# Performance work log

Hardware: AMD Instinct MI355X
Metric: run time of the kernel (lower is better)

## Reference

```python
import jax, jax.numpy as jnp
import numpy as np
import math

B, S, D = 1, 4096, 1024
H = 16
HD = D // H  # 64
MUP_SCALE = math.sqrt(1024 / 1024)  # mup_base_d_model defaults to d_in -> 1.0
ROPE_BASE = 10000.0


def apply_rope(x):
    # x: [B, H, S, HD], interleaved-pair RoPE (torchtune style)
    s, hd = x.shape[-2], x.shape[-1]
    inv_freq = 1.0 / (ROPE_BASE ** (jnp.arange(0, hd, 2, dtype=jnp.float32) / hd))  # [HD/2]
    ang = jnp.arange(s, dtype=jnp.float32)[:, None] * inv_freq[None, :]  # [S, HD/2]
    cos, sin = jnp.cos(ang), jnp.sin(ang)
    xp = x.reshape(*x.shape[:-1], hd // 2, 2)  # [..., HD/2, 2]
    x1, x2 = xp[..., 0], xp[..., 1]
    r1 = x1 * cos - x2 * sin
    r2 = x1 * sin + x2 * cos
    return jnp.stack([r1, r2], axis=-1).reshape(x.shape).astype(x.dtype)


def setup_inputs() -> dict:
    key = jax.random.key(0)
    ks = jax.random.split(key, 6)
    std = 1.0 / math.sqrt(D)
    x = jax.random.normal(ks[0], (B, S, D), dtype=jnp.float32)
    Wq = jax.random.normal(ks[1], (D, D), dtype=jnp.float32) * std  # torch layout [d_out, d_in]
    Wk = jax.random.normal(ks[2], (D, D), dtype=jnp.float32) * std
    Wv = jax.random.normal(ks[3], (D, D), dtype=jnp.float32) * std
    Wo = jax.random.normal(ks[4], (D, D), dtype=jnp.float32) * std
    bo = jnp.zeros((D,), dtype=jnp.float32)
    return {"x": x, "Wq": Wq, "Wk": Wk, "Wv": Wv, "Wo": Wo, "bo": bo}


def reference(x, Wq, Wk, Wv, Wo, bo):
    b, s, _ = x.shape
    q = jnp.einsum('bsd,ed->bse', x, Wq).reshape(b, s, H, HD).transpose(0, 2, 1, 3)
    k = jnp.einsum('bsd,ed->bse', x, Wk).reshape(b, s, H, HD).transpose(0, 2, 1, 3)
    v = jnp.einsum('bsd,ed->bse', x, Wv).reshape(b, s, H, HD).transpose(0, 2, 1, 3)
    q = apply_rope(q)
    k = apply_rope(k)
    scale = math.sqrt(HD) * MUP_SCALE
    scores = jnp.einsum('bhqd,bhkd->bhqk', q, k) / scale  # [B,H,S,S]
    causal = jnp.tril(jnp.ones((s, s), dtype=bool))
    scores = jnp.where(causal, scores, -jnp.inf)
    attn = jax.nn.softmax(scores, axis=-1)  # dropout p=0.0 -> identity
    ctx = jnp.einsum('bhqk,bhkd->bhqd', attn, v)
    ctx = ctx.transpose(0, 2, 1, 3).reshape(b, s, D)
    return jnp.einsum('bsd,ed->bse', ctx, Wo) + bo
```

## Files before the change

kernel.cpp:

```cpp
#include <hip/hip_runtime.h>
#include <hip/hip_bf16.h>

typedef __hip_bfloat16 bf16;
typedef unsigned short u16;
typedef unsigned int u32;
typedef float f32x4 __attribute__((ext_vector_type(4)));
typedef float f32x16 __attribute__((ext_vector_type(16)));
typedef __bf16 bf16x8 __attribute__((ext_vector_type(8)));
typedef u16 u16x8 __attribute__((ext_vector_type(8)));

#define DMODEL 1024
#define NH 16
#define HD 64
#define QK_LD 2048
#define SLEN 4096

typedef __attribute__((address_space(1))) const void* as1_cvp;
typedef __attribute__((address_space(3))) void* as3_vp;

__device__ __forceinline__ void gload_lds16(const void* g, void* l) {
  __builtin_amdgcn_global_load_lds((as1_cvp)g, (as3_vp)l, 16, 0, 0);
}

__device__ __forceinline__ f32x4 mfma16(bf16x8 a, bf16x8 b, f32x4 c) {
  return __builtin_amdgcn_mfma_f32_16x16x32_bf16(a, b, c, 0, 0, 0);
}
__device__ __forceinline__ f32x16 mfma32(bf16x8 a, bf16x8 b, f32x16 c) {
  return __builtin_amdgcn_mfma_f32_32x32x16_bf16(a, b, c, 0, 0, 0);
}

__device__ __forceinline__ float fexp2(float x) {
#if __has_builtin(__builtin_amdgcn_exp2f)
  return __builtin_amdgcn_exp2f(x);
#else
  return __expf(x * 0.6931471805599453f);
#endif
}

__device__ __forceinline__ u16 f2b(float f) {
  union { bf16 b; u16 s; } u; u.b = __float2bfloat16(f); return u.s;
}
__device__ __forceinline__ u32 pkbf(float a, float b) {
  union { __hip_bfloat162 h; u32 u; } cv;
  cv.h = __float22bfloat162_rn(make_float2(a, b));
  return cv.u;
}

__global__ __launch_bounds__(256) void cvt_kernel(const float* __restrict__ src,
                                                  bf16* __restrict__ dst, int n) {
  int i = (blockIdx.x * 256 + threadIdx.x) * 4;
  if (i >= n) return;
  float4 v = *(const float4*)(src + i);
  union { ushort4 u; bf16 h[4]; } o;
  o.h[0] = __float2bfloat16(v.x);
  o.h[1] = __float2bfloat16(v.y);
  o.h[2] = __float2bfloat16(v.z);
  o.h[3] = __float2bfloat16(v.w);
  *(ushort4*)(dst + i) = o.u;
}

__global__ __launch_bounds__(256) void rope_kernel(bf16* __restrict__ qk) {
  int idx = blockIdx.x * 256 + threadIdx.x;
  int p = idx & 511;
  int s = (idx >> 9) & 4095;
  int region = idx >> 21;
  int i = p & 31;
  int h = p >> 5;
  long base = (long)s * QK_LD + region * DMODEL + h * HD + 2 * i;
  float x1 = __bfloat162float(qk[base]);
  float x2 = __bfloat162float(qk[base + 1]);
  float invf = powf(10000.0f, -(float)(2 * i) / 64.0f);
  float ang = (float)s * invf;
  float sn, cs;
  sincosf(ang, &sn, &cs);
  float scale = (region == 0) ? 0.18033688011112042f : 1.0f;
  float r1 = (x1 * cs - x2 * sn) * scale;
  float r2 = (x1 * sn + x2 * cs) * scale;
  qk[base]     = __float2bfloat16(r1);
  qk[base + 1] = __float2bfloat16(r2);
}

template <int OUT_BF16>
__global__ __launch_bounds__(256) void gemm_bt(const bf16* __restrict__ A,
                                               const bf16* __restrict__ B,
                                               void* __restrict__ Cout,
                                               const float* __restrict__ bias,
                                               int M, int N, int K) {
  __shared__ __align__(16) bf16 As[128 * 32];
  __shared__ __align__(16) bf16 Bs[128 * 32];
  const int tid = threadIdx.x;
  const int lane = tid & 63;
  const int wid = tid >> 6;
  const int brow = blockIdx.y * 128;
  const int bcol = blockIdx.x * 128;
  const int wr = wid >> 1, wc = wid & 1;

  f32x4 acc[4][4] = {};

  const int srow = lane >> 2;
  const int scol = (lane & 3) * 8;
  const bf16* Ag = A + (long)(brow + wid * 32 + srow) * K + scol;
  const bf16* Bg = B + (long)(bcol + wid * 32 + srow) * K + scol;
  bf16* AsW = As + wid * 32 * 32;
  bf16* BsW = Bs + wid * 32 * 32;
  const int kof = (lane >> 4) * 8;
  const int r16 = lane & 15;

  for (int k0 = 0; k0 < K; k0 += 32) {
    __syncthreads();
    gload_lds16(Ag + k0, AsW);
    gload_lds16(Ag + k0 + (long)16 * K, AsW + 16 * 32);
    gload_lds16(Bg + k0, BsW);
    gload_lds16(Bg + k0 + (long)16 * K, BsW + 16 * 32);
    __syncthreads();
    bf16x8 af[4], bfr[4];
#pragma unroll
    for (int m = 0; m < 4; ++m)
      af[m] = *(const bf16x8*)(As + (wr * 64 + m * 16 + r16) * 32 + kof);
#pragma unroll
    for (int n = 0; n < 4; ++n)
      bfr[n] = *(const bf16x8*)(Bs + (wc * 64 + n * 16 + r16) * 32 + kof);
#pragma unroll
    for (int m = 0; m < 4; ++m)
#pragma unroll
      for (int n = 0; n < 4; ++n)
        acc[m][n] = mfma16(af[m], bfr[n], acc[m][n]);
  }

  const int r0 = (lane >> 4) * 4;
#pragma unroll
  for (int m = 0; m < 4; ++m) {
#pragma unroll
    for (int n = 0; n < 4; ++n) {
      int row = brow + wr * 64 + m * 16 + r0;
      int col = bcol + wc * 64 + n * 16 + r16;
#pragma unroll
      for (int r = 0; r < 4; ++r) {
        if (OUT_BF16) {
          ((bf16*)Cout)[(long)(row + r) * N + col] = __float2bfloat16(acc[m][n][r]);
        } else {
          ((float*)Cout)[(long)(row + r) * N + col] = acc[m][n][r] + bias[col];
        }
      }
    }
  }
}

__global__ __launch_bounds__(256, 4) void attn_kernel(const bf16* __restrict__ qk,
                                                      const bf16* __restrict__ vt,
                                                      bf16* __restrict__ ctx) {
  __shared__ __align__(16) bf16 smem[16384];
  bf16 (*Ks)[64][64] = (bf16(*)[64][64])(smem);
  bf16 (*Vt)[64][64] = (bf16(*)[64][64])(smem + 8192);

  const int tid = threadIdx.x;
  const int lane = tid & 63;
  const int wid = tid >> 6;
  const int hi = lane >> 5;
  const int l31 = lane & 31;
  const int t = blockIdx.x >> 4;
  const int h = blockIdx.x & 15;
  const int p = wid & 1;
  const int qblk = (wid < 2) ? (127 - t) : t;
  const int q0w = qblk * 32;
  const long kcol = DMODEL + (long)h * HD;

  bf16x8 qf[4];
  {
    const bf16* qp = qk + (long)(q0w + l31) * QK_LD + h * HD + hi * 8;
#pragma unroll
    for (int kt = 0; kt < 4; ++kt) qf[kt] = *(const bf16x8*)(qp + kt * 16);
  }

  const int kOff = ((lane & 7) ^ (lane >> 3)) * 8;
  const int lr = lane >> 3;
  const int srowp = (lr & 3) + 8 * (lr >> 2);

  int kro[4];
#pragma unroll
  for (int kt = 0; kt < 4; ++kt)
    kro[kt] = l31 * 64 + ((((kt << 1) | hi) ^ (l31 & 7)) * 8);
  const int vbase = l31 * 64;
  const int vslotx = l31 & 7;

  const bf16* vth = vt + (long)h * HD * SLEN;

  f32x16 acc[2] = {};
  float m_r = -1e30f, l_r = 0.0f;

  const int nkb = (129 - t) >> 1;
  const int vR = lane >> 3;

  {
#pragma unroll
    for (int c2 = 0; c2 < 2; ++c2) {
      const int c = wid * 2 + c2;
      const int sub = c >> 2, cc = c & 3;
      gload_lds16(qk + (long)(sub * 32 + srowp + 4 * (cc & 1) + 16 * (cc >> 1)) * QK_LD + kcol + kOff,
                  &Ks[0][c * 8][0]);
    }
#pragma unroll
    for (int c2 = 0; c2 < 2; ++c2) {
      const int d0 = wid * 16 + c2 * 8;
      gload_lds16(vth + (long)(d0 + vR) * SLEN + kOff, &Vt[0][d0][0]);
    }
  }

  for (int kb = 0; kb < nkb; ++kb) {
    const int cur = kb & 1;
    const int kvs = kb * 64 + p * 32;
    const bool pre = (kb + 1 < nkb);
    __syncthreads();

    if (pre) {
      const long kvn = (long)(kb + 1) * 64;
#pragma unroll
      for (int c2 = 0; c2 < 2; ++c2) {
        const int c = wid * 2 + c2;
        const int sub = c >> 2, cc = c & 3;
        gload_lds16(qk + (kvn + sub * 32 + srowp + 4 * (cc & 1) + 16 * (cc >> 1)) * QK_LD + kcol + kOff,
                    &Ks[cur ^ 1][c * 8][0]);
      }
#pragma unroll
      for (int c2 = 0; c2 < 2; ++c2) {
        const int d0 = wid * 16 + c2 * 8;
        gload_lds16(vth + (long)(d0 + vR) * SLEN + kvn + kOff, &Vt[cur ^ 1][d0][0]);
      }
    }

    if (kvs <= q0w + 31) {
      const bf16* KsC = &Ks[cur][0][0];
      const bf16* VtC = &Vt[cur][0][0];

      f32x16 c16 = {};
      __builtin_amdgcn_s_setprio(1);
#pragma unroll
      for (int kt = 0; kt < 4; ++kt) {
        bf16x8 kf = *(const bf16x8*)(KsC + p * 2048 + kro[kt]);
        c16 = mfma32(kf, qf[kt], c16);
      }
      __builtin_amdgcn_s_setprio(0);

      if (kvs + 31 > q0w) {
        const int q = q0w + l31;
        const int kvb = kvs + 8 * hi;
#pragma unroll
        for (int r = 0; r < 16; ++r) {
          int kv = kvb + (r & 3) + 4 * ((r >> 2) & 1) + 16 * (r >> 3);
          if (kv > q) c16[r] = -1e30f;
        }
      }

      float x0 = fmaxf(fmaxf(c16[0], c16[1]), fmaxf(c16[2], c16[3]));
      float x1 = fmaxf(fmaxf(c16[4], c16[5]), fmaxf(c16[6], c16[7]));
      float x2 = fmaxf(fmaxf(c16[8], c16[9]), fmaxf(c16[10], c16[11]));
      float x3 = fmaxf(fmaxf(c16[12], c16[13]), fmaxf(c16[14], c16[15]));
      float pmax = fmaxf(fmaxf(x0, x1), fmaxf(x2, x3));
      pmax = fmaxf(pmax, __shfl_xor(pmax, 32, 64));

      if (!__all(pmax <= m_r + 11.0f)) {
        float mn = fmaxf(m_r, pmax);
        float al = fexp2(m_r - mn);
        m_r = mn;
        l_r *= al;
#pragma unroll
        for (int dt = 0; dt < 2; ++dt)
#pragma unroll
          for (int r = 0; r < 16; ++r) acc[dt][r] *= al;
      }

      float pa[16];
#pragma unroll
      for (int r = 0; r < 16; ++r) pa[r] = fexp2(c16[r] - m_r);
      float rs = ((pa[0] + pa[1]) + (pa[2] + pa[3])) + ((pa[4] + pa[5]) + (pa[6] + pa[7])) +
                 (((pa[8] + pa[9]) + (pa[10] + pa[11])) + ((pa[12] + pa[13]) + (pa[14] + pa[15])));
      l_r += rs;

      union BP { u32 u[4]; bf16x8 v; } f0, f1;
      f0.u[0] = pkbf(pa[0], pa[1]);   f0.u[1] = pkbf(pa[2], pa[3]);
      f0.u[2] = pkbf(pa[4], pa[5]);   f0.u[3] = pkbf(pa[6], pa[7]);
      f1.u[0] = pkbf(pa[8], pa[9]);   f1.u[1] = pkbf(pa[10], pa[11]);
      f1.u[2] = pkbf(pa[12], pa[13]); f1.u[3] = pkbf(pa[14], pa[15]);

      __builtin_amdgcn_s_setprio(1);
#pragma unroll
      for (int dt = 0; dt < 2; ++dt) {
        const bf16* vrow = VtC + dt * 2048 + vbase;
        bf16x8 v0 = *(const bf16x8*)(vrow + (((p * 4 + hi) ^ vslotx) * 8));
        acc[dt] = mfma32(v0, f0.v, acc[dt]);
        bf16x8 v1 = *(const bf16x8*)(vrow + (((p * 4 + 2 + hi) ^ vslotx) * 8));
        acc[dt] = mfma32(v1, f1.v, acc[dt]);
      }
      __builtin_amdgcn_s_setprio(0);
    }
  }

  __syncthreads();
  float* fs = (float*)smem;
  if (wid & 1) {
    float* mb = fs + (wid >> 1) * 2176 + lane * 34;
#pragma unroll
    for (int dt = 0; dt < 2; ++dt)
#pragma unroll
      for (int r = 0; r < 16; ++r) mb[dt * 16 + r] = acc[dt][r];
    mb[32] = m_r;
    mb[33] = l_r;
  }
  __syncthreads();
  if (!(wid & 1)) {
    const float* mb = fs + (wid >> 1) * 2176 + lane * 34;
    float m1 = mb[32], l1 = mb[33];
    float ms = fmaxf(m_r, m1);
    float e0 = fexp2(m_r - ms), e1 = fexp2(m1 - ms);
    l_r = l_r * e0 + l1 * e1;
#pragma unroll
    for (int dt = 0; dt < 2; ++dt)
#pragma unroll
      for (int r = 0; r < 16; ++r)
        acc[dt][r] = acc[dt][r] * e0 + mb[dt * 16 + r] * e1;

    const float l_tot = l_r + __shfl_xor(l_r, 32, 64);
    const float inv = 1.0f / l_tot;
    bf16* scr = smem + 10240 + (wid >> 1) * 2176;
#pragma unroll
    for (int dt = 0; dt < 2; ++dt)
#pragma unroll
      for (int g2 = 0; g2 < 4; ++g2) {
        union { u16 hh[4]; unsigned long long q8; } pk4;
#pragma unroll
        for (int j = 0; j < 4; ++j) pk4.hh[j] = f2b(acc[dt][g2 * 4 + j] * inv);
        *(unsigned long long*)(scr + l31 * 68 + dt * 32 + g2 * 8 + 4 * hi) = pk4.q8;
      }
  }
  __syncthreads();
  if (!(wid & 1)) {
    const bf16* scr = smem + 10240 + (wid >> 1) * 2176;
    const int qe = lane >> 1, he = lane & 1;
    u16* cp = (u16*)ctx + (long)(q0w + qe) * DMODEL + h * HD + he * 32;
#pragma unroll
    for (int j = 0; j < 4; ++j) {
      u16x8 v = *(const u16x8*)(scr + qe * 68 + he * 32 + j * 8);
      *(u16x8*)(cp + j * 8) = v;
    }
  }
}

extern "C" void kernel_launch(void* const* d_in, const int* in_sizes, int n_in,
                              void* d_out, int out_size, void* d_ws, size_t ws_size,
                              hipStream_t stream) {
  (void)in_sizes; (void)n_in; (void)out_size; (void)ws_size;
  const float* x  = (const float*)d_in[0];
  const float* Wq = (const float*)d_in[1];
  const float* Wk = (const float*)d_in[2];
  const float* Wv = (const float*)d_in[3];
  const float* Wo = (const float*)d_in[4];
  const float* bo = (const float*)d_in[5];
  float* out = (float*)d_out;

  char* ws = (char*)d_ws;
  bf16* xb  = (bf16*)(ws);
  bf16* wqk = (bf16*)(ws + 8388608);
  bf16* wvb = (bf16*)(ws + 12582912);
  bf16* wob = (bf16*)(ws + 14680064);
  bf16* qkb = (bf16*)(ws + 16777216);
  bf16* vtb = (bf16*)(ws + 33554432);
  bf16* ctxb = (bf16*)(ws + 41943040);

  cvt_kernel<<<dim3(4096), dim3(256), 0, stream>>>(x, xb, 4194304);
  cvt_kernel<<<dim3(1024), dim3(256), 0, stream>>>(Wq, wqk, 1048576);
  cvt_kernel<<<dim3(1024), dim3(256), 0, stream>>>(Wk, wqk + 1048576, 1048576);
  cvt_kernel<<<dim3(1024), dim3(256), 0, stream>>>(Wv, wvb, 1048576);
  cvt_kernel<<<dim3(1024), dim3(256), 0, stream>>>(Wo, wob, 1048576);

  gemm_bt<1><<<dim3(16, 32), dim3(256), 0, stream>>>(xb, wqk, (void*)qkb, nullptr,
                                                     4096, 2048, 1024);
  gemm_bt<1><<<dim3(32, 8), dim3(256), 0, stream>>>(wvb, xb, (void*)vtb, nullptr,
                                                    1024, 4096, 1024);
  rope_kernel<<<dim3(16384), dim3(256), 0, stream>>>(qkb);
  attn_kernel<<<dim3(1024), dim3(256), 0, stream>>>(qkb, vtb, ctxb);
  gemm_bt<0><<<dim3(8, 32), dim3(256), 0, stream>>>(ctxb, wob, (void*)out, bo,
                                                    4096, 1024, 1024);
}
```

Baseline: 190.8 us.

## Merge convert and QKV GEMM launches, vectorize RoPE with precomputed trig table

Result: faster. 156.4 us (-18.0%).

```diff
diff --git a/kernel.cpp b/kernel.cpp
--- a/kernel.cpp
+++ b/kernel.cpp
@@ -46,10 +46,28 @@
   return cv.u;
 }
 
-__global__ __launch_bounds__(256) void cvt_kernel(const float* __restrict__ src,
-                                                  bf16* __restrict__ dst, int n) {
-  int i = (blockIdx.x * 256 + threadIdx.x) * 4;
-  if (i >= n) return;
+__global__ __launch_bounds__(256) void cvt5_kernel(const float* __restrict__ x,
+                                                   const float* __restrict__ wq,
+                                                   const float* __restrict__ wk,
+                                                   const float* __restrict__ wv,
+                                                   const float* __restrict__ wo,
+                                                   bf16* __restrict__ xb,
+                                                   bf16* __restrict__ wqk,
+                                                   bf16* __restrict__ wvb,
+                                                   bf16* __restrict__ wob) {
+  int bid = blockIdx.x;
+  const float* src; bf16* dst; long off;
+  if (bid < 4096) {
+    src = x; dst = xb; off = (long)bid * 1024;
+  } else {
+    int w = (bid - 4096) >> 10;
+    off = (long)((bid - 4096) & 1023) * 1024;
+    if (w == 0)      { src = wq; dst = wqk; }
+    else if (w == 1) { src = wk; dst = wqk + 1048576; }
+    else if (w == 2) { src = wv; dst = wvb; }
+    else             { src = wo; dst = wob; }
+  }
+  long i = off + threadIdx.x * 4;
   float4 v = *(const float4*)(src + i);
   union { ushort4 u; bf16 h[4]; } o;
   o.h[0] = __float2bfloat16(v.x);
@@ -59,25 +77,39 @@
   *(ushort4*)(dst + i) = o.u;
 }
 
-__global__ __launch_bounds__(256) void rope_kernel(bf16* __restrict__ qk) {
+__global__ __launch_bounds__(256) void trig_kernel(float2* __restrict__ tab) {
   int idx = blockIdx.x * 256 + threadIdx.x;
-  int p = idx & 511;
-  int s = (idx >> 9) & 4095;
-  int region = idx >> 21;
-  int i = p & 31;
-  int h = p >> 5;
-  long base = (long)s * QK_LD + region * DMODEL + h * HD + 2 * i;
-  float x1 = __bfloat162float(qk[base]);
-  float x2 = __bfloat162float(qk[base + 1]);
+  int s = idx >> 5, i = idx & 31;
   float invf = powf(10000.0f, -(float)(2 * i) / 64.0f);
   float ang = (float)s * invf;
   float sn, cs;
   sincosf(ang, &sn, &cs);
-  float scale = (region == 0) ? 0.18033688011112042f : 1.0f;
-  float r1 = (x1 * cs - x2 * sn) * scale;
-  float r2 = (x1 * sn + x2 * cs) * scale;
-  qk[base]     = __float2bfloat16(r1);
-  qk[base + 1] = __float2bfloat16(r2);
+  tab[idx] = make_float2(cs, sn);
+}
+
+__global__ __launch_bounds__(256) void rope_kernel(bf16* __restrict__ qk,
+                                                   const float2* __restrict__ tab) {
+  long e = (long)(blockIdx.x * 256 + threadIdx.x) * 8;
+  int s = (int)(e >> 11);
+  int col = (int)(e & 2047);
+  int i0 = (col & 63) >> 1;
+  float scale = (col < 1024) ? 0.18033688011112042f : 1.0f;
+  u16x8 v = *(const u16x8*)((const u16*)qk + e);
+  const float4* tp = (const float4*)(tab + s * 32 + i0);
+  float4 t0 = tp[0], t1 = tp[1];
+  float cs[4] = {t0.x, t0.z, t1.x, t1.z};
+  float sn[4] = {t0.y, t0.w, t1.y, t1.w};
+  u16x8 o;
+#pragma unroll
+  for (int j = 0; j < 4; ++j) {
+    union { u16 s; bf16 b; } a1, a2;
+    a1.s = v[2 * j]; a2.s = v[2 * j + 1];
+    float x1 = __bfloat162float(a1.b);
+    float x2 = __bfloat162float(a2.b);
+    o[2 * j]     = f2b((x1 * cs[j] - x2 * sn[j]) * scale);
+    o[2 * j + 1] = f2b((x1 * sn[j] + x2 * cs[j]) * scale);
+  }
+  *(u16x8*)((u16*)qk + e) = o;
 }
 
 template <int OUT_BF16>
@@ -146,6 +178,74 @@
   }
 }
 
+__global__ __launch_bounds__(256) void gemm_qkv(const bf16* __restrict__ xb,
+                                                const bf16* __restrict__ wqk,
+                                                const bf16* __restrict__ wvb,
+                                                bf16* __restrict__ qkb,
+                                                bf16* __restrict__ vtb) {
+  const int bid = blockIdx.x;
+  const bf16 *A, *B;
+  bf16* C;
+  int N, bx, by;
+  if (bid < 512) { A = xb;  B = wqk; C = qkb; N = 2048; bx = bid & 15; by = bid >> 4; }
+  else { int r = bid - 512; A = wvb; B = xb;  C = vtb; N = 4096; bx = r & 31; by = r >> 5; }
+  const int K = 1024;
+
+  __shared__ __align__(16) bf16 As[128 * 32];
+  __shared__ __align__(16) bf16 Bs[128 * 32];
+  const int tid = threadIdx.x;
+  const int lane = tid & 63;
+  const int wid = tid >> 6;
+  const int brow = by * 128;
+  const int bcol = bx * 128;
+  const int wr = wid >> 1, wc = wid & 1;
+
+  f32x4 acc[4][4] = {};
+
+  const int srow = lane >> 2;
+  const int scol = (lane & 3) * 8;
+  const bf16* Ag = A + (long)(brow + wid * 32 + srow) * K + scol;
+  const bf16* Bg = B + (long)(bcol + wid * 32 + srow) * K + scol;
+  bf16* AsW = As + wid * 32 * 32;
+  bf16* BsW = Bs + wid * 32 * 32;
+  const int kof = (lane >> 4) * 8;
+  const int r16 = lane & 15;
+
+  for (int k0 = 0; k0 < K; k0 += 32) {
+    __syncthreads();
+    gload_lds16(Ag + k0, AsW);
+    gload_lds16(Ag + k0 + (long)16 * K, AsW + 16 * 32);
+    gload_lds16(Bg + k0, BsW);
+    gload_lds16(Bg + k0 + (long)16 * K, BsW + 16 * 32);
+    __syncthreads();
+    bf16x8 af[4], bfr[4];
+#pragma unroll
+    for (int m = 0; m < 4; ++m)
+      af[m] = *(const bf16x8*)(As + (wr * 64 + m * 16 + r16) * 32 + kof);
+#pragma unroll
+    for (int n = 0; n < 4; ++n)
+      bfr[n] = *(const bf16x8*)(Bs + (wc * 64 + n * 16 + r16) * 32 + kof);
+#pragma unroll
+    for (int m = 0; m < 4; ++m)
+#pragma unroll
+      for (int n = 0; n < 4; ++n)
+        acc[m][n] = mfma16(af[m], bfr[n], acc[m][n]);
+  }
+
+  const int r0 = (lane >> 4) * 4;
+#pragma unroll
+  for (int m = 0; m < 4; ++m) {
+#pragma unroll
+    for (int n = 0; n < 4; ++n) {
+      int row = brow + wr * 64 + m * 16 + r0;
+      int col = bcol + wc * 64 + n * 16 + r16;
+#pragma unroll
+      for (int r = 0; r < 4; ++r)
+        C[(long)(row + r) * N + col] = __float2bfloat16(acc[m][n][r]);
+    }
+  }
+}
+
 __global__ __launch_bounds__(256, 4) void attn_kernel(const bf16* __restrict__ qk,
                                                       const bf16* __restrict__ vt,
                                                       bf16* __restrict__ ctx) {
@@ -365,18 +465,13 @@
   bf16* qkb = (bf16*)(ws + 16777216);
   bf16* vtb = (bf16*)(ws + 33554432);
   bf16* ctxb = (bf16*)(ws + 41943040);
-
-  cvt_kernel<<<dim3(4096), dim3(256), 0, stream>>>(x, xb, 4194304);
-  cvt_kernel<<<dim3(1024), dim3(256), 0, stream>>>(Wq, wqk, 1048576);
-  cvt_kernel<<<dim3(1024), dim3(256), 0, stream>>>(Wk, wqk + 1048576, 1048576);
-  cvt_kernel<<<dim3(1024), dim3(256), 0, stream>>>(Wv, wvb, 1048576);
-  cvt_kernel<<<dim3(1024), dim3(256), 0, stream>>>(Wo, wob, 1048576);
-
-  gemm_bt<1><<<dim3(16, 32), dim3(256), 0, stream>>>(xb, wqk, (void*)qkb, nullptr,
-                                                     4096, 2048, 1024);
-  gemm_bt<1><<<dim3(32, 8), dim3(256), 0, stream>>>(wvb, xb, (void*)vtb, nullptr,
-                                                    1024, 4096, 1024);
-  rope_kernel<<<dim3(16384), dim3(256), 0, stream>>>(qkb);
+  float2* tab = (float2*)(ws + 50331648);
+
+  trig_kernel<<<dim3(512), dim3(256), 0, stream>>>(tab);
+  cvt5_kernel<<<dim3(8192), dim3(256), 0, stream>>>(x, Wq, Wk, Wv, Wo,
+                                                    xb, wqk, wvb, wob);
+  gemm_qkv<<<dim3(768), dim3(256), 0, stream>>>(xb, wqk, wvb, qkb, vtb);
+  rope_kernel<<<dim3(4096), dim3(256), 0, stream>>>(qkb, tab);
   attn_kernel<<<dim3(1024), dim3(256), 0, stream>>>(qkb, vtb, ctxb);
   gemm_bt<0><<<dim3(8, 32), dim3(256), 0, stream>>>(ctxb, wob, (void*)out, bo,
                                                     4096, 1024, 1024);
```
